# Kernel optimization log

Measured on AMD Instinct MI355X. Metric: run time of the kernel, lower is better.

The kernel has to match this reference:

```python
import jax, jax.numpy as jnp
import numpy as np

D = 512
H = 8
DH = D // H
SPK = 4
HG = 128  # max(16, D//4)
EPS = 1e-5


def _layernorm(x, gamma, beta):
    mu = jnp.mean(x, axis=-1, keepdims=True)
    var = jnp.var(x, axis=-1, keepdims=True)
    return (x - mu) * jax.lax.rsqrt(var + EPS) * gamma + beta


def setup_inputs() -> dict:
    key = jax.random.key(0)
    ks = jax.random.split(key, 16)
    B, T = 8, 4096
    s = 0.02
    return {
        'token_emb': jax.random.normal(ks[0], (B, T, D), jnp.float32),
        'speaker_emb': jax.random.normal(ks[1], (B, D), jnp.float32),
        'We': jax.random.normal(ks[2], (D * SPK, D), jnp.float32) * s,
        'be': jnp.zeros((D * SPK,), jnp.float32),
        'spk_pos': jax.random.normal(ks[3], (1, SPK, D), jnp.float32) * s,
        'Wq': jax.random.normal(ks[4], (D, D), jnp.float32) * s,
        'bq': jnp.zeros((D,), jnp.float32),
        'Wk': jax.random.normal(ks[5], (D, D), jnp.float32) * s,
        'bk': jnp.zeros((D,), jnp.float32),
        'Wv': jax.random.normal(ks[6], (D, D), jnp.float32) * s,
        'bv': jnp.zeros((D,), jnp.float32),
        'Wo': jax.random.normal(ks[7], (D, D), jnp.float32) * s,
        'bo': jnp.zeros((D,), jnp.float32),
        'gln_gamma': jnp.ones((D,), jnp.float32),
        'gln_beta': jnp.zeros((D,), jnp.float32),
        'Wg1': jax.random.normal(ks[8], (HG, D), jnp.float32) * s,
        'bg1': jnp.zeros((HG,), jnp.float32),
        'Wg2': jax.random.normal(ks[9], (1, HG), jnp.float32) * s,
        'bg2': jnp.zeros((1,), jnp.float32),
        'ln_gamma': jnp.ones((D,), jnp.float32),
        'ln_beta': jnp.zeros((D,), jnp.float32),
    }


def reference(token_emb, speaker_emb, We, be, spk_pos, Wq, bq, Wk, bk, Wv, bv,
              Wo, bo, gln_gamma, gln_beta, Wg1, bg1, Wg2, bg2, ln_gamma, ln_beta):
    B, T, _ = token_emb.shape
    # speaker expansion: (B,D) -> (B, SPK*D) -> (B,SPK,D), plus learned pos
    spk_tokens = jax.nn.relu(speaker_emb @ We.T + be).reshape(B, SPK, D) + spk_pos
    # multi-head cross-attention (batch_first, eval-mode dropout = identity)
    q = (token_emb @ Wq.T + bq).reshape(B, T, H, DH)
    k = (spk_tokens @ Wk.T + bk).reshape(B, SPK, H, DH)
    v = (spk_tokens @ Wv.T + bv).reshape(B, SPK, H, DH)
    scores = jnp.einsum('bthd,bshd->bhts', q, k) / jnp.sqrt(jnp.float32(DH))
    w = jax.nn.softmax(scores, axis=-1)  # (B,H,T,SPK)
    ctx = jnp.einsum('bhts,bshd->bthd', w, v).reshape(B, T, D)
    attn_output = ctx @ Wo.T + bo
    attn_weights = jnp.mean(w, axis=1)  # torch MHA averages heads -> (B,T,SPK)
    # gate: LN -> Linear -> ReLU -> Linear -> Sigmoid
    g = _layernorm(token_emb, gln_gamma, gln_beta)
    g = jax.nn.relu(g @ Wg1.T + bg1)
    g_used = jax.nn.sigmoid(g @ Wg2.T + bg2)  # (B,T,1)
    # residual + final LayerNorm (dropout identity in eval)
    fused = _layernorm(token_emb + g_used * attn_output, ln_gamma, ln_beta)
    return (fused, attn_weights, g_used)
```

## Files before the change

### kernel.cpp

```cpp
#include <hip/hip_runtime.h>
#include <hip/hip_bf16.h>
#include <stdint.h>

typedef __attribute__((ext_vector_type(8))) short short8;
typedef __attribute__((ext_vector_type(4))) short short4v;
typedef __attribute__((ext_vector_type(4))) float f32x4;
typedef __attribute__((ext_vector_type(2))) unsigned int uint2v;

#define DD 512
#define TT 32
#define TN 4096
#define NB 8

__device__ __forceinline__ unsigned short f2bf(float f){
  uint32_t u = __float_as_uint(f);
  u += 0x7FFFu + ((u >> 16) & 1u);
  return (unsigned short)(u >> 16);
}
__device__ __forceinline__ float bf2f(unsigned short h){
  return __uint_as_float(((uint32_t)h) << 16);
}


__global__ void prep_spk(const float* __restrict__ se, const float* __restrict__ We,
                         const float* __restrict__ be, const float* __restrict__ spos,
                         const float* __restrict__ Wg1,
                         const float* __restrict__ glng, const float* __restrict__ glnb,
                         const float* __restrict__ bg1,
                         float* __restrict__ spk, unsigned short* __restrict__ wg1S,
                         float* __restrict__ e1, float* __restrict__ e2){
  int idx = blockIdx.x * 256 + threadIdx.x;
  if (idx < 262144){
    int sub = idx & 15; int out = idx >> 4;
    int b = out & 7, od = out >> 3;
    const float* wr = We + (size_t)od * DD + sub * 4;
    const float* sb = se + b * DD + sub * 4;
    float acc = 0.f;
#pragma unroll
    for (int i = 0; i < 8; i++){
      float4 w = *(const float4*)(wr + i * 64);
      float4 x = *(const float4*)(sb + i * 64);
      acc += w.x * x.x + w.y * x.y + w.z * x.z + w.w * x.w;
    }
    acc += __shfl_xor(acc, 1); acc += __shfl_xor(acc, 2);
    acc += __shfl_xor(acc, 4); acc += __shfl_xor(acc, 8);
    if (sub == 0) spk[b * 2048 + od] = fmaxf(acc + be[od], 0.f) + spos[od];
  } else if (idx < 327680){
    int t = idx - 262144;
    int col = t >> 9, d = t & 511;
    int nt = col >> 4, c16 = col & 15;
    int kt = d >> 5, kgp = (d >> 3) & 3, e = d & 7;
    wg1S[(size_t)(nt * 16 + kt) * 512 + (kgp * 16 + c16) * 8 + e] = f2bf(Wg1[t] * glng[d]);
  } else if (idx < 327808){
    int col = idx - 327680;
    const float* wr = Wg1 + (size_t)col * DD;
    float a1 = 0.f, a2 = 0.f;
    for (int d = 0; d < DD; d += 4){
      float4 w  = *(const float4*)(wr + d);
      float4 gm = *(const float4*)(glng + d);
      float4 bt = *(const float4*)(glnb + d);
      a1 += w.x * gm.x + w.y * gm.y + w.z * gm.z + w.w * gm.w;
      a2 += w.x * bt.x + w.y * bt.y + w.z * bt.z + w.w * bt.w;
    }
    e1[col] = a1; e2[col] = a2 + bg1[col];
  }
}

__global__ void prep_kv(const float* __restrict__ spk, const float* __restrict__ Wk,
                        const float* __restrict__ bk, const float* __restrict__ Wv,
                        const float* __restrict__ bv, float* __restrict__ kb,
                        float* __restrict__ vb){
  int idx = blockIdx.x * 256 + threadIdx.x;
  int sub = idx & 15; int out = idx >> 4;
  int hd = out >> 5; int r = out & 31; int b = r >> 2, s = r & 3;
  const float* sp  = spk + (b * 4 + s) * DD + sub * 4;
  const float* wkr = Wk + (size_t)hd * DD + sub * 4;
  const float* wvr = Wv + (size_t)hd * DD + sub * 4;
  float ak = 0.f, av = 0.f;
#pragma unroll
  for (int i = 0; i < 8; i++){
    float4 x  = *(const float4*)(sp + i * 64);
    float4 wk = *(const float4*)(wkr + i * 64);
    float4 wv = *(const float4*)(wvr + i * 64);
    ak += x.x * wk.x + x.y * wk.y + x.z * wk.z + x.w * wk.w;
    av += x.x * wv.x + x.y * wv.y + x.z * wv.z + x.w * wv.w;
  }
  ak += __shfl_xor(ak, 1); ak += __shfl_xor(ak, 2);
  ak += __shfl_xor(ak, 4); ak += __shfl_xor(ak, 8);
  av += __shfl_xor(av, 1); av += __shfl_xor(av, 2);
  av += __shfl_xor(av, 4); av += __shfl_xor(av, 8);
  if (sub == 0){
    kb[(b * 4 + s) * DD + hd] = ak + bk[hd];
    vb[(b * 4 + s) * DD + hd] = av + bv[hd];
  }
}

__global__ void prep_mu(const float* __restrict__ kb, const float* __restrict__ vb,
                        const float* __restrict__ Wq, const float* __restrict__ bq,
                        const float* __restrict__ Wo, const float* __restrict__ bo,
                        unsigned short* __restrict__ mS, unsigned short* __restrict__ uS,
                        float* __restrict__ cArr){
  int idx = blockIdx.x * 256 + threadIdx.x;
  if (idx < 32768){
    int dc = idx & 127, j = (idx >> 7) & 31, b = idx >> 12;
    int h = j >> 2, s = j & 3;
    const int d0 = dc * 4;
    const float* kr = kb + (b * 4 + s) * DD + h * 64;
    const float* wqb = Wq + (size_t)(h * 64) * DD + d0;
    float4 acc = {0.f, 0.f, 0.f, 0.f};
#pragma unroll 8
    for (int dh = 0; dh < 64; ++dh){
      float4 w4 = *(const float4*)(wqb + (size_t)dh * DD);
      float kvv = kr[dh];
      acc.x += kvv * w4.x; acc.y += kvv * w4.y;
      acc.z += kvv * w4.z; acc.w += kvv * w4.w;
    }
    const int kt = d0 >> 5, kgp = (d0 >> 3) & 3, e0 = d0 & 7, half = j >> 4;
    unsigned short* dst = mS + (size_t)(b * 16 + kt) * 1024 + half * 512 +
                          (kgp * 16 + (j & 15)) * 8 + e0;
    short4v st;
    st[0] = (short)f2bf(acc.x); st[1] = (short)f2bf(acc.y);
    st[2] = (short)f2bf(acc.z); st[3] = (short)f2bf(acc.w);
    *(short4v*)dst = st;
  } else if (idx < 163840){
    int t = idx - 32768;
    int j = t & 31; int d = (t >> 5) & 511; int b = t >> 14;
    int h = j >> 2, s = j & 3;
    const float* vr = vb + (b * 4 + s) * DD + h * 64;
    const float* wo = Wo + (size_t)d * DD + h * 64;
    float acc = 0.f;
#pragma unroll 8
    for (int dh = 0; dh < 64; dh += 4){
      float4 v4 = *(const float4*)(vr + dh);
      float4 w4 = *(const float4*)(wo + dh);
      acc += v4.x * w4.x + v4.y * w4.y + v4.z * w4.z + v4.w * w4.w;
    }
    int nc = d >> 7, nt = (d >> 4) & 7, r16p = d & 15;
    int kgp = j >> 3, e = j & 7;
    uS[(size_t)(b * 32 + nc * 8 + nt) * 512 + (kgp * 16 + r16p) * 8 + e] =
        f2bf(acc + bo[d] * 0.125f);
  } else if (idx < 164096){
    int t = idx - 163840; int j = t & 31, b = t >> 5;
    int h = j >> 2, s = j & 3;
    const float* kr = kb + (b * 4 + s) * DD + h * 64;
    const float* bqp = bq + h * 64;
    float acc = 0.f;
    for (int dh = 0; dh < 64; dh++) acc += bqp[dh] * kr[dh];
    cArr[b * 32 + j] = acc;
  }
}


__global__ __launch_bounds__(256, 2) void fused_main(
    const float* __restrict__ xin,
    const float* __restrict__ e1v, const float* __restrict__ e2v,
    const float* __restrict__ wg2v, const float* __restrict__ bg2v,
    const float* __restrict__ lng, const float* __restrict__ lnb,
    const unsigned short* __restrict__ mS,
    const unsigned short* __restrict__ uS,
    const float* __restrict__ cArr,
    const unsigned short* __restrict__ wg1S,
    float* __restrict__ outF, float* __restrict__ outAW, float* __restrict__ outG)
{
  __shared__ __align__(16) unsigned short Yb[TT * DD];
  __shared__ __align__(16) unsigned short Wl[TT * 32];
  __shared__ float smu[TT], srs[TT];
  __shared__ float aws[2][TT * 4];
  __shared__ float gp[4][TT];
  __shared__ float pp[4][TT], qq[4][TT];

  const int tid  = threadIdx.x;
  const int w    = tid >> 6;
  const int lane = tid & 63;
  const int r16  = lane & 15;
  const int kg   = lane >> 4;
  const int bb   = blockIdx.x >> 7;
  const int t0   = (blockIdx.x & 127) << 5;
  const size_t rowbase = (size_t)bb * TN + t0;
  const int swzS = (r16 & 7) << 3;

  const float* xbase = xin + rowbase * DD;
#pragma unroll
  for (int i = 0; i < 8; ++i){
    const int rr = w * 8 + i;
    const int swz = (rr & 7) << 3;
    float s = 0.f, q = 0.f;
#pragma unroll
    for (int h2 = 0; h2 < 2; ++h2){
      const int col = h2 * 256 + lane * 4;
      float4 v4 = *(const float4*)(xbase + rr * DD + col);
      short4v pk;
      pk[0] = (short)f2bf(v4.x); pk[1] = (short)f2bf(v4.y);
      pk[2] = (short)f2bf(v4.z); pk[3] = (short)f2bf(v4.w);
      s += (v4.x + v4.y) + (v4.z + v4.w);
      q += (v4.x*v4.x + v4.y*v4.y) + (v4.z*v4.z + v4.w*v4.w);
      *(short4v*)&Yb[rr * DD + (col ^ swz)] = pk;
    }
#pragma unroll
    for (int off = 1; off < 64; off <<= 1){ s += __shfl_xor(s, off); q += __shfl_xor(q, off); }
    if (lane == 0){
      const float mu = s * (1.f/DD);
      smu[rr] = mu;
      srs[rr] = rsqrtf(q * (1.f/DD) - mu*mu + 1e-5f);
    }
  }
  __syncthreads();

  const int half = w & 1;
  const int nt0  = w * 2;
  const unsigned short* mSp  = mS + (size_t)bb * 16384 + half * 512 + lane * 8;
  const unsigned short* wgp0 = wg1S + (size_t)(nt0 * 16) * 512 + lane * 8;
  const unsigned short* wgp1 = wgp0 + (size_t)16 * 512;
  f32x4 sa0 = {0.f,0.f,0.f,0.f}, sa1 = {0.f,0.f,0.f,0.f};
  f32x4 ga00 = {0.f,0.f,0.f,0.f}, ga01 = {0.f,0.f,0.f,0.f};
  f32x4 ga10 = {0.f,0.f,0.f,0.f}, ga11 = {0.f,0.f,0.f,0.f};
  if (w < 2){
#pragma unroll
    for (int kt = 0; kt < 16; ++kt){
      const int cofs = (kt*32 + kg*8) ^ swzS;
      short8 af0 = *(const short8*)&Yb[r16 * DD + cofs];
      short8 af1 = *(const short8*)&Yb[(16 + r16) * DD + cofs];
      short8 bm  = *(const short8*)(mSp + (size_t)kt * 1024);
      sa0 = __builtin_amdgcn_mfma_f32_16x16x32_bf16(af0, bm, sa0, 0, 0, 0);
      sa1 = __builtin_amdgcn_mfma_f32_16x16x32_bf16(af1, bm, sa1, 0, 0, 0);
      short8 wf0 = *(const short8*)(wgp0 + (size_t)kt * 512);
      short8 wf1 = *(const short8*)(wgp1 + (size_t)kt * 512);
      ga00 = __builtin_amdgcn_mfma_f32_16x16x32_bf16(wf0, af0, ga00, 0, 0, 0);
      ga01 = __builtin_amdgcn_mfma_f32_16x16x32_bf16(wf0, af1, ga01, 0, 0, 0);
      ga10 = __builtin_amdgcn_mfma_f32_16x16x32_bf16(wf1, af0, ga10, 0, 0, 0);
      ga11 = __builtin_amdgcn_mfma_f32_16x16x32_bf16(wf1, af1, ga11, 0, 0, 0);
    }
  } else {
#pragma unroll
    for (int kt = 0; kt < 16; ++kt){
      const int cofs = (kt*32 + kg*8) ^ swzS;
      short8 af0 = *(const short8*)&Yb[r16 * DD + cofs];
      short8 af1 = *(const short8*)&Yb[(16 + r16) * DD + cofs];
      short8 wf0 = *(const short8*)(wgp0 + (size_t)kt * 512);
      short8 wf1 = *(const short8*)(wgp1 + (size_t)kt * 512);
      ga00 = __builtin_amdgcn_mfma_f32_16x16x32_bf16(wf0, af0, ga00, 0, 0, 0);
      ga01 = __builtin_amdgcn_mfma_f32_16x16x32_bf16(wf0, af1, ga01, 0, 0, 0);
      ga10 = __builtin_amdgcn_mfma_f32_16x16x32_bf16(wf1, af0, ga10, 0, 0, 0);
      ga11 = __builtin_amdgcn_mfma_f32_16x16x32_bf16(wf1, af1, ga11, 0, 0, 0);
    }
  }

  float4 e1c[2], e2c[2], w2c[2];
#pragma unroll
  for (int t = 0; t < 2; ++t){
    const int c4 = (nt0 + t) * 16 + kg * 4;
    e1c[t] = *(const float4*)(e1v + c4);
    e2c[t] = *(const float4*)(e2v + c4);
    w2c[t] = *(const float4*)(wg2v + c4);
  }
  float4 lgh[2], lbh[2];
#pragma unroll
  for (int h2 = 0; h2 < 2; ++h2){
    lgh[h2] = *(const float4*)(lng + h2*256 + lane*4);
    lbh[h2] = *(const float4*)(lnb + h2*256 + lane*4);
  }
  const float bg2s = bg2v[0];

  if (w < 2){
    const float cv = cArr[bb*32 + half*16 + r16];
#pragma unroll
    for (int rg = 0; rg < 2; ++rg){
      const f32x4 sa = rg ? sa1 : sa0;
#pragma unroll
      for (int r = 0; r < 4; ++r){
        float s0 = (sa[r] + cv) * 0.125f;
        float mx = fmaxf(s0, __shfl_xor(s0, 1)); mx = fmaxf(mx, __shfl_xor(mx, 2));
        float e0 = __expf(s0 - mx);
        float d0 = e0; d0 += __shfl_xor(d0, 1); d0 += __shfl_xor(d0, 2);
        float wv = e0 / d0;
        float t = wv; t += __shfl_xor(t, 4); t += __shfl_xor(t, 8);
        const int rw = rg * 16 + kg * 4 + r;
        Wl[rw * 32 + half * 16 + r16] = f2bf(wv);
        if ((lane & 12) == 0) aws[half][rw * 4 + (lane & 3)] = t;
      }
    }
  }

#pragma unroll
  for (int rg = 0; rg < 2; ++rg){
    const int tk = rg * 16 + r16;
    const float mu_t = smu[tk], rs_t = srs[tk];
    float part = 0.f;
#pragma unroll
    for (int t = 0; t < 2; ++t){
      const f32x4 ga = t ? (rg ? ga11 : ga10) : (rg ? ga01 : ga00);
      float ea[4] = {e1c[t].x, e1c[t].y, e1c[t].z, e1c[t].w};
      float eb[4] = {e2c[t].x, e2c[t].y, e2c[t].z, e2c[t].w};
      float wc[4] = {w2c[t].x, w2c[t].y, w2c[t].z, w2c[t].w};
#pragma unroll
      for (int r = 0; r < 4; ++r){
        float gv = rs_t * (ga[r] - mu_t * ea[r]) + eb[r];
        part += fmaxf(gv, 0.f) * wc[r];
      }
    }
    part += __shfl_xor(part, 16); part += __shfl_xor(part, 32);
    if (kg == 0) gp[w][tk] = part;
  }
  __syncthreads();

  if (w == 2){
#pragma unroll
    for (int it = 0; it < 2; ++it){
      const int idx = it * 64 + lane;
      const int tok = idx >> 2, si = idx & 3;
      const float val = (aws[0][idx] + aws[1][idx]) * 0.125f;
      outAW[(rowbase + tok) * 4 + si] = val;
    }
  }
  float g_loc[2];
#pragma unroll
  for (int rg = 0; rg < 2; ++rg){
    const int tk = rg * 16 + r16;
    const float gs = gp[0][tk] + gp[1][tk] + gp[2][tk] + gp[3][tk];
    g_loc[rg] = 1.f / (1.f + __expf(-(gs + bg2s)));
    if (w == 3 && kg == 0) outG[rowbase + tk] = g_loc[rg];
  }

  const unsigned short* uSp = uS + (size_t)bb * 16384 + (size_t)(w * 8) * 512 + lane * 8;
  short8 uf[8];
#pragma unroll
  for (int nt = 0; nt < 8; ++nt) uf[nt] = *(const short8*)(uSp + (size_t)nt * 512);

#pragma unroll
  for (int rg = 0; rg < 2; ++rg){
    const int row = rg * 16 + r16;
    short8 awf = *(const short8*)&Wl[row * 32 + kg * 8];
    f32x4 acc[8];
#pragma unroll
    for (int nt = 0; nt < 8; ++nt){
      f32x4 z = {0.f,0.f,0.f,0.f};
      acc[nt] = __builtin_amdgcn_mfma_f32_16x16x32_bf16(uf[nt], awf, z, 0, 0, 0);
    }
    float psum = 0.f, psq = 0.f;
#pragma unroll
    for (int nt = 0; nt < 8; ++nt){
      const int c4 = w * 128 + nt * 16 + kg * 4;
      const int idx = row * DD + (c4 ^ swzS);
      uint2v xch = *(const uint2v*)&Yb[idx];
      unsigned int lo = xch[0], hi = xch[1];
      float y0 = bf2f((unsigned short)(lo & 0xffffu)) + g_loc[rg] * acc[nt][0];
      float y1 = bf2f((unsigned short)(lo >> 16))     + g_loc[rg] * acc[nt][1];
      float y2 = bf2f((unsigned short)(hi & 0xffffu)) + g_loc[rg] * acc[nt][2];
      float y3 = bf2f((unsigned short)(hi >> 16))     + g_loc[rg] * acc[nt][3];
      psum += (y0 + y1) + (y2 + y3);
      psq  += (y0*y0 + y1*y1) + (y2*y2 + y3*y3);
      uint2v yp;
      yp[0] = (unsigned)f2bf(y0) | ((unsigned)f2bf(y1) << 16);
      yp[1] = (unsigned)f2bf(y2) | ((unsigned)f2bf(y3) << 16);
      *(uint2v*)&Yb[idx] = yp;
    }
    psum += __shfl_xor(psum, 16); psum += __shfl_xor(psum, 32);
    psq  += __shfl_xor(psq, 16);  psq  += __shfl_xor(psq, 32);
    if (kg == 0){ pp[w][row] = psum; qq[w][row] = psq; }
  }
  __syncthreads();

#pragma unroll
  for (int i = 0; i < 8; ++i){
    const int rr = w * 8 + i;
    const float sm = pp[0][rr] + pp[1][rr] + pp[2][rr] + pp[3][rr];
    const float sq = qq[0][rr] + qq[1][rr] + qq[2][rr] + qq[3][rr];
    const float mu2 = sm * (1.f/DD);
    const float rs2 = rsqrtf(sq * (1.f/DD) - mu2*mu2 + 1e-5f);
    const int swz = (rr & 7) << 3;
#pragma unroll
    for (int h2 = 0; h2 < 2; ++h2){
      const int col = h2 * 256 + lane * 4;
      short4v yv = *(const short4v*)&Yb[rr * DD + (col ^ swz)];
      float la[4] = {lgh[h2].x, lgh[h2].y, lgh[h2].z, lgh[h2].w};
      float lb4[4] = {lbh[h2].x, lbh[h2].y, lbh[h2].z, lbh[h2].w};
      float4 o;
      o.x = (bf2f((unsigned short)yv[0]) - mu2) * rs2 * la[0] + lb4[0];
      o.y = (bf2f((unsigned short)yv[1]) - mu2) * rs2 * la[1] + lb4[1];
      o.z = (bf2f((unsigned short)yv[2]) - mu2) * rs2 * la[2] + lb4[2];
      o.w = (bf2f((unsigned short)yv[3]) - mu2) * rs2 * la[3] + lb4[3];
      *(float4*)(outF + (rowbase + rr) * DD + col) = o;
    }
  }
}


extern "C" void kernel_launch(void* const* d_in, const int* in_sizes, int n_in,
                              void* d_out, int out_size, void* d_ws, size_t ws_size,
                              hipStream_t stream)
{
  const float* token = (const float*)d_in[0];
  const float* semb  = (const float*)d_in[1];
  const float* We    = (const float*)d_in[2];
  const float* be    = (const float*)d_in[3];
  const float* spos  = (const float*)d_in[4];
  const float* Wq    = (const float*)d_in[5];
  const float* bq    = (const float*)d_in[6];
  const float* Wk    = (const float*)d_in[7];
  const float* bk    = (const float*)d_in[8];
  const float* Wv    = (const float*)d_in[9];
  const float* bv    = (const float*)d_in[10];
  const float* Wo    = (const float*)d_in[11];
  const float* bo    = (const float*)d_in[12];
  const float* glng  = (const float*)d_in[13];
  const float* glnb  = (const float*)d_in[14];
  const float* Wg1   = (const float*)d_in[15];
  const float* bg1   = (const float*)d_in[16];
  const float* Wg2   = (const float*)d_in[17];
  const float* bg2   = (const float*)d_in[18];
  const float* lng   = (const float*)d_in[19];
  const float* lnb   = (const float*)d_in[20];

  char* ws = (char*)d_ws;
  float* e1             = (float*)(ws + 0);
  float* e2             = (float*)(ws + 512);
  float* spk            = (float*)(ws + 1024);
  float* kb             = (float*)(ws + 65536 + 1024);
  float* vb             = (float*)(ws + 131072 + 1024);
  unsigned short* mS    = (unsigned short*)(ws + 196608);
  unsigned short* uS    = (unsigned short*)(ws + 458752);
  float* cArr           = (float*)(ws + 720896);
  unsigned short* wg1S  = (unsigned short*)(ws + 721920);

  float* outF  = (float*)d_out;
  float* outAW = outF + (size_t)NB * TN * DD;
  float* outG  = outAW + (size_t)NB * TN * 4;

  prep_spk<<<dim3(1281), dim3(256), 0, stream>>>(semb, We, be, spos, Wg1, glng, glnb, bg1,
                                                 spk, wg1S, e1, e2);
  prep_kv<<<dim3(1024), dim3(256), 0, stream>>>(spk, Wk, bk, Wv, bv, kb, vb);
  prep_mu<<<dim3(642), dim3(256), 0, stream>>>(kb, vb, Wq, bq, Wo, bo, mS, uS, cArr);
  fused_main<<<dim3(NB * TN / TT), dim3(256), 0, stream>>>(
      token, e1, e2, Wg2, bg2, lng, lnb,
      mS, uS, cArr, wg1S, outF, outAW, outG);
}
```

Measured before the change: 65.85 us.

## Merge three prep kernels into one cooperative kernel with grid syncs

Replaces the three sequential preprocessing launches (speaker expansion, K/V projection, folded Q/O matrices) with a single cooperative kernel that uses grid-stride loops and grid.sync between stages. The aim is to remove two kernel launch gaps and their inter-kernel drain/fill overhead. In exchange it adds grid-wide barrier costs and needs all 1024 blocks to be co-resident, which the cooperative launch requires; if they cannot all fit, the launch fails.

```diff
diff --git a/kernel.cpp b/kernel.cpp
--- a/kernel.cpp
+++ b/kernel.cpp
@@ -1,6 +1,9 @@
 #include <hip/hip_runtime.h>
 #include <hip/hip_bf16.h>
+#include <hip/hip_cooperative_groups.h>
 #include <stdint.h>
+
+namespace cg = cooperative_groups;
 
 typedef __attribute__((ext_vector_type(8))) short short8;
 typedef __attribute__((ext_vector_type(4))) short short4v;
@@ -22,131 +25,137 @@
 }
 
 
-__global__ void prep_spk(const float* __restrict__ se, const float* __restrict__ We,
-                         const float* __restrict__ be, const float* __restrict__ spos,
-                         const float* __restrict__ Wg1,
-                         const float* __restrict__ glng, const float* __restrict__ glnb,
-                         const float* __restrict__ bg1,
-                         float* __restrict__ spk, unsigned short* __restrict__ wg1S,
-                         float* __restrict__ e1, float* __restrict__ e2){
-  int idx = blockIdx.x * 256 + threadIdx.x;
-  if (idx < 262144){
+__global__ __launch_bounds__(256, 4) void prep_all(
+    const float* __restrict__ se,  const float* __restrict__ We,
+    const float* __restrict__ be,  const float* __restrict__ spos,
+    const float* __restrict__ Wg1, const float* __restrict__ glng,
+    const float* __restrict__ glnb,const float* __restrict__ bg1,
+    const float* __restrict__ Wk,  const float* __restrict__ bk,
+    const float* __restrict__ Wv,  const float* __restrict__ bv,
+    const float* __restrict__ Wq,  const float* __restrict__ bq,
+    const float* __restrict__ Wo,  const float* __restrict__ bo,
+    float* __restrict__ spk, unsigned short* __restrict__ wg1S,
+    float* __restrict__ e1,  float* __restrict__ e2,
+    float* __restrict__ kb,  float* __restrict__ vb,
+    unsigned short* __restrict__ mS, unsigned short* __restrict__ uS,
+    float* __restrict__ cArr)
+{
+  cg::grid_group grid = cg::this_grid();
+  const int gsz = gridDim.x * 256;
+  const int tid0 = blockIdx.x * 256 + threadIdx.x;
+
+  for (int idx = tid0; idx < 327808; idx += gsz){
+    if (idx < 262144){
+      int sub = idx & 15; int out = idx >> 4;
+      int b = out & 7, od = out >> 3;
+      const float* wr = We + (size_t)od * DD + sub * 4;
+      const float* sb = se + b * DD + sub * 4;
+      float acc = 0.f;
+#pragma unroll
+      for (int i = 0; i < 8; i++){
+        float4 w = *(const float4*)(wr + i * 64);
+        float4 x = *(const float4*)(sb + i * 64);
+        acc += w.x * x.x + w.y * x.y + w.z * x.z + w.w * x.w;
+      }
+      acc += __shfl_xor(acc, 1); acc += __shfl_xor(acc, 2);
+      acc += __shfl_xor(acc, 4); acc += __shfl_xor(acc, 8);
+      if (sub == 0) spk[b * 2048 + od] = fmaxf(acc + be[od], 0.f) + spos[od];
+    } else if (idx < 327680){
+      int t = idx - 262144;
+      int col = t >> 9, d = t & 511;
+      int nt = col >> 4, c16 = col & 15;
+      int kt = d >> 5, kgp = (d >> 3) & 3, e = d & 7;
+      wg1S[(size_t)(nt * 16 + kt) * 512 + (kgp * 16 + c16) * 8 + e] = f2bf(Wg1[t] * glng[d]);
+    } else {
+      int col = idx - 327680;
+      const float* wr = Wg1 + (size_t)col * DD;
+      float a1 = 0.f, a2 = 0.f;
+      for (int d = 0; d < DD; d += 4){
+        float4 w  = *(const float4*)(wr + d);
+        float4 gm = *(const float4*)(glng + d);
+        float4 bt = *(const float4*)(glnb + d);
+        a1 += w.x * gm.x + w.y * gm.y + w.z * gm.z + w.w * gm.w;
+        a2 += w.x * bt.x + w.y * bt.y + w.z * bt.z + w.w * bt.w;
+      }
+      e1[col] = a1; e2[col] = a2 + bg1[col];
+    }
+  }
+  grid.sync();
+
+  for (int idx = tid0; idx < 262144; idx += gsz){
     int sub = idx & 15; int out = idx >> 4;
-    int b = out & 7, od = out >> 3;
-    const float* wr = We + (size_t)od * DD + sub * 4;
-    const float* sb = se + b * DD + sub * 4;
-    float acc = 0.f;
+    int hd = out >> 5; int r = out & 31; int b = r >> 2, s = r & 3;
+    const float* sp  = spk + (b * 4 + s) * DD + sub * 4;
+    const float* wkr = Wk + (size_t)hd * DD + sub * 4;
+    const float* wvr = Wv + (size_t)hd * DD + sub * 4;
+    float ak = 0.f, av = 0.f;
 #pragma unroll
     for (int i = 0; i < 8; i++){
-      float4 w = *(const float4*)(wr + i * 64);
-      float4 x = *(const float4*)(sb + i * 64);
-      acc += w.x * x.x + w.y * x.y + w.z * x.z + w.w * x.w;
-    }
-    acc += __shfl_xor(acc, 1); acc += __shfl_xor(acc, 2);
-    acc += __shfl_xor(acc, 4); acc += __shfl_xor(acc, 8);
-    if (sub == 0) spk[b * 2048 + od] = fmaxf(acc + be[od], 0.f) + spos[od];
-  } else if (idx < 327680){
-    int t = idx - 262144;
-    int col = t >> 9, d = t & 511;
-    int nt = col >> 4, c16 = col & 15;
-    int kt = d >> 5, kgp = (d >> 3) & 3, e = d & 7;
-    wg1S[(size_t)(nt * 16 + kt) * 512 + (kgp * 16 + c16) * 8 + e] = f2bf(Wg1[t] * glng[d]);
-  } else if (idx < 327808){
-    int col = idx - 327680;
-    const float* wr = Wg1 + (size_t)col * DD;
-    float a1 = 0.f, a2 = 0.f;
-    for (int d = 0; d < DD; d += 4){
-      float4 w  = *(const float4*)(wr + d);
-      float4 gm = *(const float4*)(glng + d);
-      float4 bt = *(const float4*)(glnb + d);
-      a1 += w.x * gm.x + w.y * gm.y + w.z * gm.z + w.w * gm.w;
-      a2 += w.x * bt.x + w.y * bt.y + w.z * bt.z + w.w * bt.w;
-    }
-    e1[col] = a1; e2[col] = a2 + bg1[col];
-  }
-}
-
-__global__ void prep_kv(const float* __restrict__ spk, const float* __restrict__ Wk,
-                        const float* __restrict__ bk, const float* __restrict__ Wv,
-                        const float* __restrict__ bv, float* __restrict__ kb,
-                        float* __restrict__ vb){
-  int idx = blockIdx.x * 256 + threadIdx.x;
-  int sub = idx & 15; int out = idx >> 4;
-  int hd = out >> 5; int r = out & 31; int b = r >> 2, s = r & 3;
-  const float* sp  = spk + (b * 4 + s) * DD + sub * 4;
-  const float* wkr = Wk + (size_t)hd * DD + sub * 4;
-  const float* wvr = Wv + (size_t)hd * DD + sub * 4;
-  float ak = 0.f, av = 0.f;
-#pragma unroll
-  for (int i = 0; i < 8; i++){
-    float4 x  = *(const float4*)(sp + i * 64);
-    float4 wk = *(const float4*)(wkr + i * 64);
-    float4 wv = *(const float4*)(wvr + i * 64);
-    ak += x.x * wk.x + x.y * wk.y + x.z * wk.z + x.w * wk.w;
-    av += x.x * wv.x + x.y * wv.y + x.z * wv.z + x.w * wv.w;
-  }
-  ak += __shfl_xor(ak, 1); ak += __shfl_xor(ak, 2);
-  ak += __shfl_xor(ak, 4); ak += __shfl_xor(ak, 8);
-  av += __shfl_xor(av, 1); av += __shfl_xor(av, 2);
-  av += __shfl_xor(av, 4); av += __shfl_xor(av, 8);
-  if (sub == 0){
-    kb[(b * 4 + s) * DD + hd] = ak + bk[hd];
-    vb[(b * 4 + s) * DD + hd] = av + bv[hd];
-  }
-}
-
-__global__ void prep_mu(const float* __restrict__ kb, const float* __restrict__ vb,
-                        const float* __restrict__ Wq, const float* __restrict__ bq,
-                        const float* __restrict__ Wo, const float* __restrict__ bo,
-                        unsigned short* __restrict__ mS, unsigned short* __restrict__ uS,
-                        float* __restrict__ cArr){
-  int idx = blockIdx.x * 256 + threadIdx.x;
-  if (idx < 32768){
-    int dc = idx & 127, j = (idx >> 7) & 31, b = idx >> 12;
-    int h = j >> 2, s = j & 3;
-    const int d0 = dc * 4;
-    const float* kr = kb + (b * 4 + s) * DD + h * 64;
-    const float* wqb = Wq + (size_t)(h * 64) * DD + d0;
-    float4 acc = {0.f, 0.f, 0.f, 0.f};
+      float4 x  = *(const float4*)(sp + i * 64);
+      float4 wk = *(const float4*)(wkr + i * 64);
+      float4 wv = *(const float4*)(wvr + i * 64);
+      ak += x.x * wk.x + x.y * wk.y + x.z * wk.z + x.w * wk.w;
+      av += x.x * wv.x + x.y * wv.y + x.z * wv.z + x.w * wv.w;
+    }
+    ak += __shfl_xor(ak, 1); ak += __shfl_xor(ak, 2);
+    ak += __shfl_xor(ak, 4); ak += __shfl_xor(ak, 8);
+    av += __shfl_xor(av, 1); av += __shfl_xor(av, 2);
+    av += __shfl_xor(av, 4); av += __shfl_xor(av, 8);
+    if (sub == 0){
+      kb[(b * 4 + s) * DD + hd] = ak + bk[hd];
+      vb[(b * 4 + s) * DD + hd] = av + bv[hd];
+    }
+  }
+  grid.sync();
+
+  for (int idx = tid0; idx < 164096; idx += gsz){
+    if (idx < 32768){
+      int dc = idx & 127, j = (idx >> 7) & 31, b = idx >> 12;
+      int h = j >> 2, s = j & 3;
+      const int d0 = dc * 4;
+      const float* kr = kb + (b * 4 + s) * DD + h * 64;
+      const float* wqb = Wq + (size_t)(h * 64) * DD + d0;
+      float4 acc = {0.f, 0.f, 0.f, 0.f};
 #pragma unroll 8
-    for (int dh = 0; dh < 64; ++dh){
-      float4 w4 = *(const float4*)(wqb + (size_t)dh * DD);
-      float kvv = kr[dh];
-      acc.x += kvv * w4.x; acc.y += kvv * w4.y;
-      acc.z += kvv * w4.z; acc.w += kvv * w4.w;
-    }
-    const int kt = d0 >> 5, kgp = (d0 >> 3) & 3, e0 = d0 & 7, half = j >> 4;
-    unsigned short* dst = mS + (size_t)(b * 16 + kt) * 1024 + half * 512 +
-                          (kgp * 16 + (j & 15)) * 8 + e0;
-    short4v st;
-    st[0] = (short)f2bf(acc.x); st[1] = (short)f2bf(acc.y);
-    st[2] = (short)f2bf(acc.z); st[3] = (short)f2bf(acc.w);
-    *(short4v*)dst = st;
-  } else if (idx < 163840){
-    int t = idx - 32768;
-    int j = t & 31; int d = (t >> 5) & 511; int b = t >> 14;
-    int h = j >> 2, s = j & 3;
-    const float* vr = vb + (b * 4 + s) * DD + h * 64;
-    const float* wo = Wo + (size_t)d * DD + h * 64;
-    float acc = 0.f;
+      for (int dh = 0; dh < 64; ++dh){
+        float4 w4 = *(const float4*)(wqb + (size_t)dh * DD);
+        float kvv = kr[dh];
+        acc.x += kvv * w4.x; acc.y += kvv * w4.y;
+        acc.z += kvv * w4.z; acc.w += kvv * w4.w;
+      }
+      const int kt = d0 >> 5, kgp = (d0 >> 3) & 3, e0 = d0 & 7, half = j >> 4;
+      unsigned short* dst = mS + (size_t)(b * 16 + kt) * 1024 + half * 512 +
+                            (kgp * 16 + (j & 15)) * 8 + e0;
+      short4v st;
+      st[0] = (short)f2bf(acc.x); st[1] = (short)f2bf(acc.y);
+      st[2] = (short)f2bf(acc.z); st[3] = (short)f2bf(acc.w);
+      *(short4v*)dst = st;
+    } else if (idx < 163840){
+      int t = idx - 32768;
+      int j = t & 31; int d = (t >> 5) & 511; int b = t >> 14;
+      int h = j >> 2, s = j & 3;
+      const float* vr = vb + (b * 4 + s) * DD + h * 64;
+      const float* wo = Wo + (size_t)d * DD + h * 64;
+      float acc = 0.f;
 #pragma unroll 8
-    for (int dh = 0; dh < 64; dh += 4){
-      float4 v4 = *(const float4*)(vr + dh);
-      float4 w4 = *(const float4*)(wo + dh);
-      acc += v4.x * w4.x + v4.y * w4.y + v4.z * w4.z + v4.w * w4.w;
-    }
-    int nc = d >> 7, nt = (d >> 4) & 7, r16p = d & 15;
-    int kgp = j >> 3, e = j & 7;
-    uS[(size_t)(b * 32 + nc * 8 + nt) * 512 + (kgp * 16 + r16p) * 8 + e] =
-        f2bf(acc + bo[d] * 0.125f);
-  } else if (idx < 164096){
-    int t = idx - 163840; int j = t & 31, b = t >> 5;
-    int h = j >> 2, s = j & 3;
-    const float* kr = kb + (b * 4 + s) * DD + h * 64;
-    const float* bqp = bq + h * 64;
-    float acc = 0.f;
-    for (int dh = 0; dh < 64; dh++) acc += bqp[dh] * kr[dh];
-    cArr[b * 32 + j] = acc;
+      for (int dh = 0; dh < 64; dh += 4){
+        float4 v4 = *(const float4*)(vr + dh);
+        float4 w4 = *(const float4*)(wo + dh);
+        acc += v4.x * w4.x + v4.y * w4.y + v4.z * w4.z + v4.w * w4.w;
+      }
+      int nc = d >> 7, nt = (d >> 4) & 7, r16p = d & 15;
+      int kgp = j >> 3, e = j & 7;
+      uS[(size_t)(b * 32 + nc * 8 + nt) * 512 + (kgp * 16 + r16p) * 8 + e] =
+          f2bf(acc + bo[d] * 0.125f);
+    } else {
+      int t = idx - 163840; int j = t & 31, b = t >> 5;
+      int h = j >> 2, s = j & 3;
+      const float* kr = kb + (b * 4 + s) * DD + h * 64;
+      const float* bqp = bq + h * 64;
+      float acc = 0.f;
+      for (int dh = 0; dh < 64; dh++) acc += bqp[dh] * kr[dh];
+      cArr[b * 32 + j] = acc;
+    }
   }
 }
 
@@ -426,10 +435,17 @@
   float* outAW = outF + (size_t)NB * TN * DD;
   float* outG  = outAW + (size_t)NB * TN * 4;
 
-  prep_spk<<<dim3(1281), dim3(256), 0, stream>>>(semb, We, be, spos, Wg1, glng, glnb, bg1,
-                                                 spk, wg1S, e1, e2);
-  prep_kv<<<dim3(1024), dim3(256), 0, stream>>>(spk, Wk, bk, Wv, bv, kb, vb);
-  prep_mu<<<dim3(642), dim3(256), 0, stream>>>(kb, vb, Wq, bq, Wo, bo, mS, uS, cArr);
+  void* args[] = {
+    (void*)&semb, (void*)&We, (void*)&be, (void*)&spos,
+    (void*)&Wg1, (void*)&glng, (void*)&glnb, (void*)&bg1,
+    (void*)&Wk, (void*)&bk, (void*)&Wv, (void*)&bv,
+    (void*)&Wq, (void*)&bq, (void*)&Wo, (void*)&bo,
+    (void*)&spk, (void*)&wg1S, (void*)&e1, (void*)&e2,
+    (void*)&kb, (void*)&vb, (void*)&mS, (void*)&uS, (void*)&cArr
+  };
+  hipLaunchCooperativeKernel((const void*)prep_all, dim3(1024), dim3(256),
+                             args, 0, stream);
+
   fused_main<<<dim3(NB * TN / TT), dim3(256), 0, stream>>>(
       token, e1, e2, Wg2, bg2, lng, lnb,
       mS, uS, cArr, wg1S, outF, outAW, outG);
```

Result: slower. 240.1 us (+264.6%).

## Double token tile to 64 rows with 512-thread blocks in fused kernel

Applied to the files above, without the earlier changes.

Raises the per-block token tile from 32 to 64 rows and the block size from 256 to 512 threads (8 waves). Work is redistributed so each wave handles one 16-column slice of the gate weights across four row groups and a 64-column slice of the output projection. Each Wg1/uS weight fragment loaded from global memory is now reused across four row groups instead of two, cutting weight traffic per token. The cost is a 64 KB LDS tile per block and higher register pressure under the 512,4 launch bound, which may reduce occupancy or cause spills.

```diff
diff --git a/kernel.cpp b/kernel.cpp
--- a/kernel.cpp
+++ b/kernel.cpp
@@ -8,7 +8,7 @@
 typedef __attribute__((ext_vector_type(2))) unsigned int uint2v;
 
 #define DD 512
-#define TT 32
+#define TT 64
 #define TN 4096
 #define NB 8
 
@@ -151,7 +151,7 @@
 }
 
 
-__global__ __launch_bounds__(256, 2) void fused_main(
+__global__ __launch_bounds__(512, 4) void fused_main(
     const float* __restrict__ xin,
     const float* __restrict__ e1v, const float* __restrict__ e2v,
     const float* __restrict__ wg2v, const float* __restrict__ bg2v,
@@ -166,16 +166,16 @@
   __shared__ __align__(16) unsigned short Wl[TT * 32];
   __shared__ float smu[TT], srs[TT];
   __shared__ float aws[2][TT * 4];
-  __shared__ float gp[4][TT];
-  __shared__ float pp[4][TT], qq[4][TT];
+  __shared__ float gp[8][TT];
+  __shared__ float pp[8][TT], qq[8][TT];
 
   const int tid  = threadIdx.x;
   const int w    = tid >> 6;
   const int lane = tid & 63;
   const int r16  = lane & 15;
   const int kg   = lane >> 4;
-  const int bb   = blockIdx.x >> 7;
-  const int t0   = (blockIdx.x & 127) << 5;
+  const int bb   = blockIdx.x >> 6;
+  const int t0   = (blockIdx.x & 63) << 6;
   const size_t rowbase = (size_t)bb * TN + t0;
   const int swzS = (r16 & 7) << 3;
 
@@ -206,52 +206,62 @@
   }
   __syncthreads();
 
-  const int half = w & 1;
-  const int nt0  = w * 2;
-  const unsigned short* mSp  = mS + (size_t)bb * 16384 + half * 512 + lane * 8;
-  const unsigned short* wgp0 = wg1S + (size_t)(nt0 * 16) * 512 + lane * 8;
-  const unsigned short* wgp1 = wgp0 + (size_t)16 * 512;
-  f32x4 sa0 = {0.f,0.f,0.f,0.f}, sa1 = {0.f,0.f,0.f,0.f};
-  f32x4 ga00 = {0.f,0.f,0.f,0.f}, ga01 = {0.f,0.f,0.f,0.f};
-  f32x4 ga10 = {0.f,0.f,0.f,0.f}, ga11 = {0.f,0.f,0.f,0.f};
-  if (w < 2){
+  const int half   = w >> 1;
+  const int rgpair = w & 1;
+  const int rgA = rgpair * 2, rgB = rgpair * 2 + 1;
+  const unsigned short* mSp = mS + (size_t)bb * 16384 + half * 512 + lane * 8;
+  const unsigned short* wgp = wg1S + (size_t)(w * 16) * 512 + lane * 8;
+
+  f32x4 saA = {0.f,0.f,0.f,0.f}, saB = {0.f,0.f,0.f,0.f};
+  f32x4 ga[4];
+#pragma unroll
+  for (int rg = 0; rg < 4; ++rg){ f32x4 z = {0.f,0.f,0.f,0.f}; ga[rg] = z; }
+
+  if (w < 4){
 #pragma unroll
     for (int kt = 0; kt < 16; ++kt){
       const int cofs = (kt*32 + kg*8) ^ swzS;
-      short8 af0 = *(const short8*)&Yb[r16 * DD + cofs];
+      short8 af0 = *(const short8*)&Yb[( 0 + r16) * DD + cofs];
       short8 af1 = *(const short8*)&Yb[(16 + r16) * DD + cofs];
-      short8 bm  = *(const short8*)(mSp + (size_t)kt * 1024);
-      sa0 = __builtin_amdgcn_mfma_f32_16x16x32_bf16(af0, bm, sa0, 0, 0, 0);
-      sa1 = __builtin_amdgcn_mfma_f32_16x16x32_bf16(af1, bm, sa1, 0, 0, 0);
-      short8 wf0 = *(const short8*)(wgp0 + (size_t)kt * 512);
-      short8 wf1 = *(const short8*)(wgp1 + (size_t)kt * 512);
-      ga00 = __builtin_amdgcn_mfma_f32_16x16x32_bf16(wf0, af0, ga00, 0, 0, 0);
-      ga01 = __builtin_amdgcn_mfma_f32_16x16x32_bf16(wf0, af1, ga01, 0, 0, 0);
-      ga10 = __builtin_amdgcn_mfma_f32_16x16x32_bf16(wf1, af0, ga10, 0, 0, 0);
-      ga11 = __builtin_amdgcn_mfma_f32_16x16x32_bf16(wf1, af1, ga11, 0, 0, 0);
+      short8 af2 = *(const short8*)&Yb[(32 + r16) * DD + cofs];
+      short8 af3 = *(const short8*)&Yb[(48 + r16) * DD + cofs];
+      short8 bm = *(const short8*)(mSp + (size_t)kt * 1024);
+      short8 afA = rgpair ? af2 : af0;
+      short8 afB = rgpair ? af3 : af1;
+      saA = __builtin_amdgcn_mfma_f32_16x16x32_bf16(afA, bm, saA, 0, 0, 0);
+      saB = __builtin_amdgcn_mfma_f32_16x16x32_bf16(afB, bm, saB, 0, 0, 0);
+      short8 wf = *(const short8*)(wgp + (size_t)kt * 512);
+      ga[0] = __builtin_amdgcn_mfma_f32_16x16x32_bf16(wf, af0, ga[0], 0, 0, 0);
+      ga[1] = __builtin_amdgcn_mfma_f32_16x16x32_bf16(wf, af1, ga[1], 0, 0, 0);
+      ga[2] = __builtin_amdgcn_mfma_f32_16x16x32_bf16(wf, af2, ga[2], 0, 0, 0);
+      ga[3] = __builtin_amdgcn_mfma_f32_16x16x32_bf16(wf, af3, ga[3], 0, 0, 0);
     }
   } else {
 #pragma unroll
     for (int kt = 0; kt < 16; ++kt){
       const int cofs = (kt*32 + kg*8) ^ swzS;
-      short8 af0 = *(const short8*)&Yb[r16 * DD + cofs];
+      short8 af0 = *(const short8*)&Yb[( 0 + r16) * DD + cofs];
       short8 af1 = *(const short8*)&Yb[(16 + r16) * DD + cofs];
-      short8 wf0 = *(const short8*)(wgp0 + (size_t)kt * 512);
-      short8 wf1 = *(const short8*)(wgp1 + (size_t)kt * 512);
-      ga00 = __builtin_amdgcn_mfma_f32_16x16x32_bf16(wf0, af0, ga00, 0, 0, 0);
-      ga01 = __builtin_amdgcn_mfma_f32_16x16x32_bf16(wf0, af1, ga01, 0, 0, 0);
-      ga10 = __builtin_amdgcn_mfma_f32_16x16x32_bf16(wf1, af0, ga10, 0, 0, 0);
-      ga11 = __builtin_amdgcn_mfma_f32_16x16x32_bf16(wf1, af1, ga11, 0, 0, 0);
-    }
-  }
-
-  float4 e1c[2], e2c[2], w2c[2];
-#pragma unroll
-  for (int t = 0; t < 2; ++t){
-    const int c4 = (nt0 + t) * 16 + kg * 4;
-    e1c[t] = *(const float4*)(e1v + c4);
-    e2c[t] = *(const float4*)(e2v + c4);
-    w2c[t] = *(const float4*)(wg2v + c4);
+      short8 af2 = *(const short8*)&Yb[(32 + r16) * DD + cofs];
+      short8 af3 = *(const short8*)&Yb[(48 + r16) * DD + cofs];
+      short8 wf = *(const short8*)(wgp + (size_t)kt * 512);
+      ga[0] = __builtin_amdgcn_mfma_f32_16x16x32_bf16(wf, af0, ga[0], 0, 0, 0);
+      ga[1] = __builtin_amdgcn_mfma_f32_16x16x32_bf16(wf, af1, ga[1], 0, 0, 0);
+      ga[2] = __builtin_amdgcn_mfma_f32_16x16x32_bf16(wf, af2, ga[2], 0, 0, 0);
+      ga[3] = __builtin_amdgcn_mfma_f32_16x16x32_bf16(wf, af3, ga[3], 0, 0, 0);
+    }
+  }
+
+  const unsigned short* uSp = uS + (size_t)bb * 16384 + (size_t)(w * 4) * 512 + lane * 8;
+  short8 uf[4];
+#pragma unroll
+  for (int l = 0; l < 4; ++l) uf[l] = *(const short8*)(uSp + (size_t)l * 512);
+  float4 e1c, e2c, w2c;
+  {
+    const int c4 = w * 16 + kg * 4;
+    e1c = *(const float4*)(e1v + c4);
+    e2c = *(const float4*)(e2v + c4);
+    w2c = *(const float4*)(wg2v + c4);
   }
   float4 lgh[2], lbh[2];
 #pragma unroll
@@ -261,11 +271,12 @@
   }
   const float bg2s = bg2v[0];
 
-  if (w < 2){
+  if (w < 4){
     const float cv = cArr[bb*32 + half*16 + r16];
 #pragma unroll
-    for (int rg = 0; rg < 2; ++rg){
-      const f32x4 sa = rg ? sa1 : sa0;
+    for (int t2 = 0; t2 < 2; ++t2){
+      const f32x4 sa = t2 ? saB : saA;
+      const int rg = t2 ? rgB : rgA;
 #pragma unroll
       for (int r = 0; r < 4; ++r){
         float s0 = (sa[r] + cv) * 0.125f;
@@ -282,71 +293,63 @@
   }
 
 #pragma unroll
-  for (int rg = 0; rg < 2; ++rg){
+  for (int rg = 0; rg < 4; ++rg){
     const int tk = rg * 16 + r16;
     const float mu_t = smu[tk], rs_t = srs[tk];
+    float ea[4] = {e1c.x, e1c.y, e1c.z, e1c.w};
+    float eb[4] = {e2c.x, e2c.y, e2c.z, e2c.w};
+    float wc[4] = {w2c.x, w2c.y, w2c.z, w2c.w};
     float part = 0.f;
 #pragma unroll
-    for (int t = 0; t < 2; ++t){
-      const f32x4 ga = t ? (rg ? ga11 : ga10) : (rg ? ga01 : ga00);
-      float ea[4] = {e1c[t].x, e1c[t].y, e1c[t].z, e1c[t].w};
-      float eb[4] = {e2c[t].x, e2c[t].y, e2c[t].z, e2c[t].w};
-      float wc[4] = {w2c[t].x, w2c[t].y, w2c[t].z, w2c[t].w};
-#pragma unroll
-      for (int r = 0; r < 4; ++r){
-        float gv = rs_t * (ga[r] - mu_t * ea[r]) + eb[r];
-        part += fmaxf(gv, 0.f) * wc[r];
-      }
+    for (int r = 0; r < 4; ++r){
+      float gv = rs_t * (ga[rg][r] - mu_t * ea[r]) + eb[r];
+      part += fmaxf(gv, 0.f) * wc[r];
     }
     part += __shfl_xor(part, 16); part += __shfl_xor(part, 32);
     if (kg == 0) gp[w][tk] = part;
   }
   __syncthreads();
 
-  if (w == 2){
-#pragma unroll
-    for (int it = 0; it < 2; ++it){
+  if (w == 4){
+#pragma unroll
+    for (int it = 0; it < 4; ++it){
       const int idx = it * 64 + lane;
       const int tok = idx >> 2, si = idx & 3;
       const float val = (aws[0][idx] + aws[1][idx]) * 0.125f;
       outAW[(rowbase + tok) * 4 + si] = val;
     }
   }
-  float g_loc[2];
-#pragma unroll
-  for (int rg = 0; rg < 2; ++rg){
+  float g_loc[4];
+#pragma unroll
+  for (int rg = 0; rg < 4; ++rg){
     const int tk = rg * 16 + r16;
-    const float gs = gp[0][tk] + gp[1][tk] + gp[2][tk] + gp[3][tk];
+    const float gs = (gp[0][tk] + gp[1][tk]) + (gp[2][tk] + gp[3][tk]) +
+                     (gp[4][tk] + gp[5][tk]) + (gp[6][tk] + gp[7][tk]);
     g_loc[rg] = 1.f / (1.f + __expf(-(gs + bg2s)));
-    if (w == 3 && kg == 0) outG[rowbase + tk] = g_loc[rg];
-  }
-
-  const unsigned short* uSp = uS + (size_t)bb * 16384 + (size_t)(w * 8) * 512 + lane * 8;
-  short8 uf[8];
-#pragma unroll
-  for (int nt = 0; nt < 8; ++nt) uf[nt] = *(const short8*)(uSp + (size_t)nt * 512);
-
-#pragma unroll
-  for (int rg = 0; rg < 2; ++rg){
+    if (w == 7 && kg == 0) outG[rowbase + tk] = g_loc[rg];
+  }
+
+#pragma unroll
+  for (int rg = 0; rg < 4; ++rg){
     const int row = rg * 16 + r16;
     short8 awf = *(const short8*)&Wl[row * 32 + kg * 8];
-    f32x4 acc[8];
-#pragma unroll
-    for (int nt = 0; nt < 8; ++nt){
+    f32x4 acc[4];
+#pragma unroll
+    for (int l = 0; l < 4; ++l){
       f32x4 z = {0.f,0.f,0.f,0.f};
-      acc[nt] = __builtin_amdgcn_mfma_f32_16x16x32_bf16(uf[nt], awf, z, 0, 0, 0);
+      acc[l] = __builtin_amdgcn_mfma_f32_16x16x32_bf16(uf[l], awf, z, 0, 0, 0);
     }
     float psum = 0.f, psq = 0.f;
 #pragma unroll
-    for (int nt = 0; nt < 8; ++nt){
-      const int c4 = w * 128 + nt * 16 + kg * 4;
+    for (int l = 0; l < 4; ++l){
+      const int c4 = w * 64 + l * 16 + kg * 4;
       const int idx = row * DD + (c4 ^ swzS);
       uint2v xch = *(const uint2v*)&Yb[idx];
       unsigned int lo = xch[0], hi = xch[1];
-      float y0 = bf2f((unsigned short)(lo & 0xffffu)) + g_loc[rg] * acc[nt][0];
-      float y1 = bf2f((unsigned short)(lo >> 16))     + g_loc[rg] * acc[nt][1];
-      float y2 = bf2f((unsigned short)(hi & 0xffffu)) + g_loc[rg] * acc[nt][2];
-      float y3 = bf2f((unsigned short)(hi >> 16))     + g_loc[rg] * acc[nt][3];
+      float y0 = bf2f((unsigned short)(lo & 0xffffu)) + g_loc[rg] * acc[l][0];
+      float y1 = bf2f((unsigned short)(lo >> 16))     + g_loc[rg] * acc[l][1];
+      float y2 = bf2f((unsigned short)(hi & 0xffffu)) + g_loc[rg] * acc[l][2];
+      float y3 = bf2f((unsigned short)(hi >> 16))     + g_loc[rg] * acc[l][3];
       psum += (y0 + y1) + (y2 + y3);
       psq  += (y0*y0 + y1*y1) + (y2*y2 + y3*y3);
       uint2v yp;
@@ -363,8 +366,10 @@
 #pragma unroll
   for (int i = 0; i < 8; ++i){
     const int rr = w * 8 + i;
-    const float sm = pp[0][rr] + pp[1][rr] + pp[2][rr] + pp[3][rr];
-    const float sq = qq[0][rr] + qq[1][rr] + qq[2][rr] + qq[3][rr];
+    const float sm = (pp[0][rr] + pp[1][rr]) + (pp[2][rr] + pp[3][rr]) +
+                     (pp[4][rr] + pp[5][rr]) + (pp[6][rr] + pp[7][rr]);
+    const float sq = (qq[0][rr] + qq[1][rr]) + (qq[2][rr] + qq[3][rr]) +
+                     (qq[4][rr] + qq[5][rr]) + (qq[6][rr] + qq[7][rr]);
     const float mu2 = sm * (1.f/DD);
     const float rs2 = rsqrtf(sq * (1.f/DD) - mu2*mu2 + 1e-5f);
     const int swz = (rr & 7) << 3;
@@ -430,7 +435,7 @@
                                                  spk, wg1S, e1, e2);
   prep_kv<<<dim3(1024), dim3(256), 0, stream>>>(spk, Wk, bk, Wv, bv, kb, vb);
   prep_mu<<<dim3(642), dim3(256), 0, stream>>>(kb, vb, Wq, bq, Wo, bo, mS, uS, cArr);
-  fused_main<<<dim3(NB * TN / TT), dim3(256), 0, stream>>>(
+  fused_main<<<dim3(NB * TN / TT), dim3(512), 0, stream>>>(
       token, e1, e2, Wg2, bg2, lng, lnb,
       mS, uS, cArr, wg1S, outF, outAW, outG);
 }
```

After: 69.34 us. 5.3% more time.
